# Kernel optimization log

Hardware: AMD Instinct MI355X
Metric: run time of the kernel (lower is better)

## Reference

```python
import jax, jax.numpy as jnp
import numpy as np

B, L, D_IN, D_MODEL, H = 8, 1024, 256, 512, 8
D_HEAD = D_MODEL // H


def setup_inputs() -> dict:
    key = jax.random.key(0)
    ks = jax.random.split(key, 12)
    queries = jax.random.normal(ks[0], (B, L, D_IN), dtype=jnp.float32)
    keys_ = jax.random.normal(ks[1], (B, L, D_IN), dtype=jnp.float32)
    values = jax.random.normal(ks[2], (B, L, D_IN), dtype=jnp.float32)
    attention_mask = jnp.ones((B, L), dtype=jnp.int32)
    # binary symmetric-ish adjacency (sparse molecular graph style)
    adjacency_matrix = (jax.random.uniform(ks[3], (B, L, L)) < 0.05).astype(jnp.float32)
    distance_matrix = jax.random.uniform(ks[4], (B, L, L), dtype=jnp.float32) * 10.0
    s = 1.0 / np.sqrt(D_IN)
    W_q = jax.random.normal(ks[5], (D_MODEL, D_IN), dtype=jnp.float32) * s
    W_k = jax.random.normal(ks[6], (D_MODEL, D_IN), dtype=jnp.float32) * s
    W_v = jax.random.normal(ks[7], (D_MODEL, D_IN), dtype=jnp.float32) * s
    W_o = jax.random.normal(ks[8], (D_MODEL, D_MODEL), dtype=jnp.float32) / np.sqrt(D_MODEL)
    lambda_a = jax.random.normal(ks[9], (H,), dtype=jnp.float32) * 0.1
    lambda_d = jax.random.normal(ks[10], (H,), dtype=jnp.float32) * 0.1
    return {"queries": queries, "keys": keys_, "values": values,
            "attention_mask": attention_mask, "adjacency_matrix": adjacency_matrix,
            "distance_matrix": distance_matrix, "W_q": W_q, "W_k": W_k,
            "W_v": W_v, "W_o": W_o, "lambda_a": lambda_a, "lambda_d": lambda_d}


def _split_heads(x):
    # (b, l, d_model) -> (b, h, l, d_head)
    b, l, _ = x.shape
    return x.reshape(b, l, H, D_HEAD).transpose(0, 2, 1, 3)


def reference(queries, keys, values, attention_mask, adjacency_matrix,
              distance_matrix, W_q, W_k, W_v, W_o, lambda_a, lambda_d):
    Q = _split_heads(queries @ W_q.T)   # (b,h,l,d)
    K = _split_heads(keys @ W_k.T)
    V = _split_heads(values @ W_v.T)
    scores = jnp.einsum("bhqd,bhkd->bhqk", Q, K) / jnp.sqrt(jnp.asarray(D_HEAD, Q.dtype))
    # MSRSA: per-head learned scalars inject graph structure into the scores
    scores = (scores
              + lambda_a[None, :, None, None] * adjacency_matrix[:, None, :, :]
              + lambda_d[None, :, None, None] * distance_matrix[:, None, :, :])
    mask = attention_mask[:, None, None, :] > 0  # (b,1,1,l) key mask
    scores = jnp.where(mask, scores, jnp.asarray(-1e9, scores.dtype))
    attn_weight = jax.nn.softmax(scores, axis=-1)  # (b,h,l,l)
    out = jnp.einsum("bhqk,bhkd->bhqd", attn_weight, V)
    out = out.transpose(0, 2, 1, 3).reshape(queries.shape[0], queries.shape[1], D_MODEL)
    return out @ W_o.T
```

## Files before the change

### kernel.cpp

```cpp
#include <hip/hip_runtime.h>
#include <hip/hip_fp16.h>

#define BB 8
#define LL 1024
#define DIN 256
#define DM 512
#define HH 8
#define DH 64

typedef __attribute__((ext_vector_type(8))) short bf16x8;
typedef __attribute__((ext_vector_type(4))) float f32x4;
typedef _Float16 h2f __attribute__((ext_vector_type(2)));

__device__ __forceinline__ unsigned short f2bf(float f) {
  union { float f; unsigned u; } c; c.f = f;
  unsigned u = c.u;
  return (unsigned short)((u + 0x7fffu + ((u >> 16) & 1u)) >> 16);
}

#if defined(__has_builtin)
#if __has_builtin(__builtin_amdgcn_cvt_pk_bf16_f32)
#define HAS_PK_BF16 1
#endif
#endif

#if defined(HAS_PK_BF16)
typedef __bf16 bf2 __attribute__((ext_vector_type(2)));
__device__ __forceinline__ unsigned pk2(float lo, float hi) {
  union { bf2 v; unsigned u; } c;
  c.v = __builtin_amdgcn_cvt_pk_bf16_f32(lo, hi);
  return c.u;
}
#else
__device__ __forceinline__ unsigned pk2(float lo, float hi) {
  return ((unsigned)f2bf(hi) << 16) | f2bf(lo);
}
#endif

__device__ __forceinline__ float biasdot(unsigned u, h2f lam, float t) {
#if defined(__HIP_DEVICE_COMPILE__)
  union { unsigned v; h2f hv; } c; c.v = u;
  return __builtin_amdgcn_fdot2(c.hv, lam, t, false);
#else
  (void)u; (void)lam;
  return t;
#endif
}

__device__ __forceinline__ unsigned pkh(float a, float d) {
  return (unsigned)__half_as_ushort(__float2half_rn(a)) |
         ((unsigned)__half_as_ushort(__float2half_rn(d)) << 16);
}

__device__ __forceinline__ void async_copy16(void* lds, const void* g) {
  __builtin_amdgcn_global_load_lds(
      (const __attribute__((address_space(1))) unsigned*)g,
      (__attribute__((address_space(3))) unsigned*)lds, 16, 0, 0);
}

__global__ __launch_bounds__(256) void prep(
    const float* __restrict__ qin, const float* __restrict__ kin,
    const float* __restrict__ vin,
    const float* __restrict__ wq, const float* __restrict__ wk,
    const float* __restrict__ wv, const float* __restrict__ wo,
    const int* __restrict__ msk,
    const float* __restrict__ adj, const float* __restrict__ dis,
    unsigned short* __restrict__ xq, unsigned short* __restrict__ xk,
    unsigned short* __restrict__ xv,
    unsigned short* __restrict__ wqb, unsigned short* __restrict__ wkb,
    unsigned short* __restrict__ wvb, unsigned short* __restrict__ wob,
    float* __restrict__ mad, unsigned* __restrict__ bp)
{
  int t = blockIdx.x * 256 + threadIdx.x;
  const int XS = 524288, WS = 32768;
  if (t < 3 * XS) {
    int seg = t >> 19, off = t & (XS - 1);
    const float* s = (seg == 0) ? qin : (seg == 1) ? kin : vin;
    unsigned short* d = (seg == 0) ? xq : (seg == 1) ? xk : xv;
    float4 f = ((const float4*)s)[off];
    uint2 o = { pk2(f.x, f.y), pk2(f.z, f.w) };
    ((uint2*)d)[off] = o;
    return;
  }
  t -= 3 * XS;
  if (t < 3 * WS) {
    int seg = t >> 15, off = t & (WS - 1);
    const float* s = (seg == 0) ? wq : (seg == 1) ? wk : wv;
    unsigned short* d = (seg == 0) ? wqb : (seg == 1) ? wkb : wvb;
    float4 f = ((const float4*)s)[off];
    uint2 o = { pk2(f.x, f.y), pk2(f.z, f.w) };
    ((uint2*)d)[off] = o;
    return;
  }
  t -= 3 * WS;
  if (t < 65536) {
    float4 f = ((const float4*)wo)[t];
    uint2 o = { pk2(f.x, f.y), pk2(f.z, f.w) };
    ((uint2*)wob)[t] = o;
    return;
  }
  t -= 65536;
  if (t < 2048) {
    int4 m = ((const int4*)msk)[t];
    float4 f = { m.x ? 0.0f : -30000.0f, m.y ? 0.0f : -30000.0f,
                 m.z ? 0.0f : -30000.0f, m.w ? 0.0f : -30000.0f };
    ((float4*)mad)[t] = f;
    return;
  }
  t -= 2048;
  float4 a4 = ((const float4*)adj)[t];
  float4 d4 = ((const float4*)dis)[t];
  uint4 o = { pkh(a4.x, d4.x), pkh(a4.y, d4.y), pkh(a4.z, d4.z), pkh(a4.w, d4.w) };
  ((uint4*)bp)[t] = o;
}

__global__ __launch_bounds__(256) void qkv_proj(
    const unsigned short* __restrict__ xq, const unsigned short* __restrict__ xk,
    const unsigned short* __restrict__ xv,
    const unsigned short* __restrict__ wqb, const unsigned short* __restrict__ wkb,
    const unsigned short* __restrict__ wvb,
    unsigned short* __restrict__ qb, unsigned short* __restrict__ kb,
    unsigned short* __restrict__ vt)
{
  const int t = blockIdx.z;
  const unsigned short* __restrict__ X = (t == 0) ? xq : (t == 1) ? xk : xv;
  const unsigned short* __restrict__ W = (t == 0) ? wqb : (t == 1) ? wkb : wvb;
  const int m0 = blockIdx.y * 128;
  const int h  = blockIdx.x;
  __shared__ __align__(16) char arena[24576];
  const int tid = threadIdx.x;
  const int wid = tid >> 6;
  const int lane = tid & 63;
  const int lo = lane & 15;
  const int quad = lane >> 4;

  f32x4 acc[2][4];
#pragma unroll
  for (int mi = 0; mi < 2; ++mi)
#pragma unroll
    for (int ni = 0; ni < 4; ++ni) acc[mi][ni] = (f32x4)0.0f;

#pragma unroll
  for (int j = 0; j < 2; ++j) {
    int id = j * 256 + tid, r = id >> 2, c = id & 3;
    async_copy16(arena + j * 4096 + wid * 1024,
                 X + (size_t)(m0 + r) * DIN + ((c ^ (r & 3)) * 8));
  }
  {
    int id = tid, r = id >> 2, c = id & 3;
    async_copy16(arena + 16384 + wid * 1024,
                 W + (size_t)(h * 64 + r) * DIN + ((c ^ (r & 3)) * 8));
  }
  __syncthreads();

  for (int it = 0; it < 8; ++it) {
    const int p = it & 1;
    if (it < 7) {
      const int kk = (it + 1) * 32, q = 1 - p;
#pragma unroll
      for (int j = 0; j < 2; ++j) {
        int id = j * 256 + tid, r = id >> 2, c = id & 3;
        async_copy16(arena + q * 8192 + j * 4096 + wid * 1024,
                     X + (size_t)(m0 + r) * DIN + kk + ((c ^ (r & 3)) * 8));
      }
      {
        int id = tid, r = id >> 2, c = id & 3;
        async_copy16(arena + 16384 + q * 4096 + wid * 1024,
                     W + (size_t)(h * 64 + r) * DIN + kk + ((c ^ (r & 3)) * 8));
      }
    }
    const unsigned short* Ab = (const unsigned short*)(arena + p * 8192);
    const unsigned short* Bb = (const unsigned short*)(arena + 16384 + p * 4096);
    bf16x8 a[2], bfr[4];
#pragma unroll
    for (int mi = 0; mi < 2; ++mi) {
      int R = wid * 32 + mi * 16 + lo;
      a[mi] = *(const bf16x8*)&Ab[R * 32 + ((quad ^ (R & 3)) * 8)];
    }
#pragma unroll
    for (int ni = 0; ni < 4; ++ni) {
      int N = ni * 16 + lo;
      bfr[ni] = *(const bf16x8*)&Bb[N * 32 + ((quad ^ (N & 3)) * 8)];
    }
#pragma unroll
    for (int mi = 0; mi < 2; ++mi)
#pragma unroll
      for (int ni = 0; ni < 4; ++ni)
        acc[mi][ni] = __builtin_amdgcn_mfma_f32_16x16x32_bf16(
            a[mi], bfr[ni], acc[mi][ni], 0, 0, 0);
    __syncthreads();
  }

  const int b = m0 >> 10;
  const int lbase0 = (m0 & 1023) + wid * 32;
  if (t < 2) {
    unsigned short* dstp = (t == 0) ? qb : kb;
#pragma unroll
    for (int mi = 0; mi < 2; ++mi)
#pragma unroll
      for (int ni = 0; ni < 4; ++ni) {
        int d = ni * 16 + lo;
#pragma unroll
        for (int r = 0; r < 4; ++r) {
          int lb = lbase0 + mi * 16 + quad * 4 + r;
          dstp[((size_t)(b * HH + h) * LL + lb) * DH + d] = f2bf(acc[mi][ni][r]);
        }
      }
  } else {
#pragma unroll
    for (int mi = 0; mi < 2; ++mi)
#pragma unroll
      for (int ni = 0; ni < 4; ++ni) {
        int d = ni * 16 + lo;
        int lb = lbase0 + mi * 16 + quad * 4;
        uint2 o = { pk2(acc[mi][ni][0], acc[mi][ni][1]),
                    pk2(acc[mi][ni][2], acc[mi][ni][3]) };
        *(uint2*)&vt[((size_t)(b * HH + h) * DH + d) * LL + lb] = o;
      }
  }
}

__global__ __launch_bounds__(256, 3) void attn(
    const unsigned short* __restrict__ qb, const unsigned short* __restrict__ kb,
    const unsigned short* __restrict__ vt,
    const float* __restrict__ mad, const unsigned* __restrict__ bp,
    const float* __restrict__ la_, const float* __restrict__ ld_,
    unsigned short* __restrict__ ao)
{
  const int bi = blockIdx.x;
  const int b  = bi & 7;
  const int hg = (bi >> 3) & 3;
  const int q0 = (bi >> 5) * 32;
  const int tid = threadIdx.x;
  const int wid = tid >> 6;
  const int lane = tid & 63;
  const int lo = lane & 15;
  const int quad = lane >> 4;
  const int h  = hg * 2 + (wid & 1);
  const int kh = wid >> 1;
  const int bh = b * HH + h;

  __shared__ __align__(16) char arena[17408];
  unsigned short* pbufw = (unsigned short*)arena + wid * 1280;
  float*          mgbuf = (float*)arena;

  const float LOG2E = 1.44269504f;
  const float la2 = la_[h] * LOG2E, ld2 = ld_[h] * LOG2E;
  const float sc2 = 0.125f * LOG2E;
  h2f lam2;
  lam2.x = (_Float16)la2;
  lam2.y = (_Float16)ld2;

  const unsigned short* qp = qb + ((size_t)bh * LL + q0) * DH;
  bf16x8 qB[2][2];
#pragma unroll
  for (int nj = 0; nj < 2; ++nj)
#pragma unroll
    for (int ki = 0; ki < 2; ++ki)
      qB[nj][ki] = *(const bf16x8*)&qp[(nj * 16 + lo) * DH + ki * 32 + quad * 8];

  const unsigned short* kp = kb + (size_t)bh * LL * DH;
  const unsigned short* vp = vt + (size_t)bh * DH * LL;
  const unsigned* bpp = bp + ((size_t)b * LL + q0) * LL;
  const float* mp = mad + b * LL;

  f32x4 o[4][2];
  float rs[2] = {0.0f, 0.0f};
#pragma unroll
  for (int md = 0; md < 4; ++md)
#pragma unroll
    for (int nj = 0; nj < 2; ++nj) o[md][nj] = (f32x4)0.0f;

  const int kbeg = kh * (LL / 2);

  bf16x8 kA0[2][2], kA1[2][2];
#pragma unroll
  for (int mi = 0; mi < 2; ++mi)
#pragma unroll
    for (int ki = 0; ki < 2; ++ki)
      kA0[mi][ki] = *(const bf16x8*)&kp[(size_t)(kbeg + mi * 16 + lo) * DH +
                                        ki * 32 + quad * 8];

#define ATTN_TILE(KC, KN, JT)                                                  \
  do {                                                                         \
    const int k0 = kbeg + (JT) * 32;                                           \
    const int kn0 = ((JT) < 15) ? (k0 + 32) : k0;   \
    uint4 ub[2][2];                                                            \
    _Pragma("unroll") for (int mi = 0; mi < 2; ++mi)                           \
      _Pragma("unroll") for (int nj = 0; nj < 2; ++nj)                         \
        ub[mi][nj] = *(const uint4*)&bpp[(size_t)(nj * 16 + lo) * LL +         \
                                         k0 + mi * 16 + quad * 4];             \
    f32x4 msv[2];                                                              \
    _Pragma("unroll") for (int mi = 0; mi < 2; ++mi)                           \
      msv[mi] = *(const f32x4*)&mp[k0 + mi * 16 + quad * 4];                   \
    bf16x8 vA[4];                                                              \
    _Pragma("unroll") for (int md = 0; md < 4; ++md)                           \
      vA[md] = *(const bf16x8*)&vp[(md * 16 + lo) * LL + k0 + quad * 8];       \
    _Pragma("unroll") for (int mi = 0; mi < 2; ++mi)                           \
      _Pragma("unroll") for (int ki = 0; ki < 2; ++ki)                         \
        KN[mi][ki] = *(const bf16x8*)&kp[(size_t)(kn0 + mi * 16 + lo) * DH +   \
                                         ki * 32 + quad * 8];                  \
    __builtin_amdgcn_sched_barrier(0);           \
    f32x4 s[2][2];                                                             \
    _Pragma("unroll") for (int mi = 0; mi < 2; ++mi)                           \
      _Pragma("unroll") for (int nj = 0; nj < 2; ++nj) s[mi][nj] = (f32x4)0.0f;\
    _Pragma("unroll") for (int ki = 0; ki < 2; ++ki)                           \
      _Pragma("unroll") for (int mi = 0; mi < 2; ++mi)                         \
        _Pragma("unroll") for (int nj = 0; nj < 2; ++nj)                       \
          s[mi][nj] = __builtin_amdgcn_mfma_f32_16x16x32_bf16(                 \
              KC[mi][ki], qB[nj][ki], s[mi][nj], 0, 0, 0);                     \
    _Pragma("unroll") for (int mi = 0; mi < 2; ++mi)                           \
      _Pragma("unroll") for (int nj = 0; nj < 2; ++nj) {                       \
        float p4[4];                                                           \
        _Pragma("unroll") for (int r = 0; r < 4; ++r) {                        \
          float tb = fmaf(s[mi][nj][r], sc2, msv[mi][r]);                      \
          p4[r] = __builtin_amdgcn_exp2f(biasdot(ub[mi][nj][r], lam2, tb));    \
        }                                                                      \
        rs[nj] += (p4[0] + p4[1]) + (p4[2] + p4[3]);                           \
        uint2 w = { pk2(p4[0], p4[1]), pk2(p4[2], p4[3]) };                    \
        *(uint2*)&pbufw[(nj * 16 + lo) * 40 + mi * 16 + quad * 4] = w;         \
      }                                                                        \
    asm volatile("s_waitcnt lgkmcnt(0)" ::: "memory");                         \
    bf16x8 pB[2];                                                              \
    _Pragma("unroll") for (int nj = 0; nj < 2; ++nj)                           \
      pB[nj] = *(const bf16x8*)&pbufw[(nj * 16 + lo) * 40 + quad * 8];         \
    _Pragma("unroll") for (int md = 0; md < 4; ++md)                           \
      _Pragma("unroll") for (int nj = 0; nj < 2; ++nj)                         \
        o[md][nj] = __builtin_amdgcn_mfma_f32_16x16x32_bf16(                   \
            vA[md], pB[nj], o[md][nj], 0, 0, 0);                               \
  } while (0)

  for (int j2 = 0; j2 < 8; ++j2) {
    ATTN_TILE(kA0, kA1, 2 * j2);
    ATTN_TILE(kA1, kA0, 2 * j2 + 1);
  }
#undef ATTN_TILE

  __syncthreads();
  const int hs = wid & 1;
  if (kh == 1) {
#pragma unroll
    for (int md = 0; md < 4; ++md)
#pragma unroll
      for (int nj = 0; nj < 2; ++nj)
#pragma unroll
        for (int r = 0; r < 4; ++r)
          mgbuf[hs * 2176 + ((md * 2 + nj) * 4 + r) * 64 + lane] = o[md][nj][r];
    mgbuf[hs * 2176 + 32 * 64 + lane] = rs[0];
    mgbuf[hs * 2176 + 33 * 64 + lane] = rs[1];
  }
  __syncthreads();
  if (kh == 0) {
#pragma unroll
    for (int md = 0; md < 4; ++md)
#pragma unroll
      for (int nj = 0; nj < 2; ++nj)
#pragma unroll
        for (int r = 0; r < 4; ++r)
          o[md][nj][r] += mgbuf[hs * 2176 + ((md * 2 + nj) * 4 + r) * 64 + lane];
    rs[0] += mgbuf[hs * 2176 + 32 * 64 + lane];
    rs[1] += mgbuf[hs * 2176 + 33 * 64 + lane];
    float inv[2];
#pragma unroll
    for (int nj = 0; nj < 2; ++nj) {
      rs[nj] += __shfl_xor(rs[nj], 16);
      rs[nj] += __shfl_xor(rs[nj], 32);
      inv[nj] = __builtin_amdgcn_rcpf(rs[nj]);
    }
#pragma unroll
    for (int md = 0; md < 4; ++md)
#pragma unroll
      for (int nj = 0; nj < 2; ++nj) {
        int l = q0 + nj * 16 + lo;
        uint2 st = { pk2(o[md][nj][0] * inv[nj], o[md][nj][1] * inv[nj]),
                     pk2(o[md][nj][2] * inv[nj], o[md][nj][3] * inv[nj]) };
        *(uint2*)&ao[((size_t)b * LL + l) * DM + h * DH + md * 16 + quad * 4] = st;
      }
  }
}

__global__ __launch_bounds__(256) void oproj(
    const unsigned short* __restrict__ ao, const unsigned short* __restrict__ wob,
    float* __restrict__ out)
{
  const int m0 = blockIdx.y * 128;
  const int n0 = blockIdx.x * 64;
  __shared__ __align__(16) char arena[24576];
  const int tid = threadIdx.x;
  const int wid = tid >> 6;
  const int lane = tid & 63;
  const int lo = lane & 15;
  const int quad = lane >> 4;

  f32x4 acc[2][4];
#pragma unroll
  for (int mi = 0; mi < 2; ++mi)
#pragma unroll
    for (int ni = 0; ni < 4; ++ni) acc[mi][ni] = (f32x4)0.0f;

#pragma unroll
  for (int j = 0; j < 2; ++j) {
    int id = j * 256 + tid, r = id >> 2, c = id & 3;
    async_copy16(arena + j * 4096 + wid * 1024,
                 ao + (size_t)(m0 + r) * DM + ((c ^ (r & 3)) * 8));
  }
  {
    int id = tid, r = id >> 2, c = id & 3;
    async_copy16(arena + 16384 + wid * 1024,
                 wob + (size_t)(n0 + r) * DM + ((c ^ (r & 3)) * 8));
  }
  __syncthreads();

  for (int it = 0; it < 16; ++it) {
    const int p = it & 1;
    if (it < 15) {
      const int kk = (it + 1) * 32, q = 1 - p;
#pragma unroll
      for (int j = 0; j < 2; ++j) {
        int id = j * 256 + tid, r = id >> 2, c = id & 3;
        async_copy16(arena + q * 8192 + j * 4096 + wid * 1024,
                     ao + (size_t)(m0 + r) * DM + kk + ((c ^ (r & 3)) * 8));
      }
      {
        int id = tid, r = id >> 2, c = id & 3;
        async_copy16(arena + 16384 + q * 4096 + wid * 1024,
                     wob + (size_t)(n0 + r) * DM + kk + ((c ^ (r & 3)) * 8));
      }
    }
    const unsigned short* Ab = (const unsigned short*)(arena + p * 8192);
    const unsigned short* Bb = (const unsigned short*)(arena + 16384 + p * 4096);
    bf16x8 a[2], bfr[4];
#pragma unroll
    for (int mi = 0; mi < 2; ++mi) {
      int R = wid * 32 + mi * 16 + lo;
      a[mi] = *(const bf16x8*)&Ab[R * 32 + ((quad ^ (R & 3)) * 8)];
    }
#pragma unroll
    for (int ni = 0; ni < 4; ++ni) {
      int N = ni * 16 + lo;
      bfr[ni] = *(const bf16x8*)&Bb[N * 32 + ((quad ^ (N & 3)) * 8)];
    }
#pragma unroll
    for (int mi = 0; mi < 2; ++mi)
#pragma unroll
      for (int ni = 0; ni < 4; ++ni)
        acc[mi][ni] = __builtin_amdgcn_mfma_f32_16x16x32_bf16(
            a[mi], bfr[ni], acc[mi][ni], 0, 0, 0);
    __syncthreads();
  }

#pragma unroll
  for (int mi = 0; mi < 2; ++mi)
#pragma unroll
    for (int ni = 0; ni < 4; ++ni)
#pragma unroll
      for (int r = 0; r < 4; ++r)
        out[(size_t)(m0 + wid * 32 + mi * 16 + quad * 4 + r) * DM +
            n0 + ni * 16 + lo] = acc[mi][ni][r];
}

extern "C" void kernel_launch(void* const* d_in, const int* in_sizes, int n_in,
                              void* d_out, int out_size, void* d_ws, size_t ws_size,
                              hipStream_t stream) {
  const float* qin = (const float*)d_in[0];
  const float* kin = (const float*)d_in[1];
  const float* vin = (const float*)d_in[2];
  const int*   msk = (const int*)d_in[3];
  const float* adj = (const float*)d_in[4];
  const float* dis = (const float*)d_in[5];
  const float* wq  = (const float*)d_in[6];
  const float* wk  = (const float*)d_in[7];
  const float* wv  = (const float*)d_in[8];
  const float* wo  = (const float*)d_in[9];
  const float* la  = (const float*)d_in[10];
  const float* ld  = (const float*)d_in[11];
  float* out = (float*)d_out;

  const size_t tensb = (size_t)BB * HH * LL * DH;
  const size_t xsz   = (size_t)BB * LL * DIN;
  unsigned short* qb  = (unsigned short*)d_ws;
  unsigned short* kb  = qb + tensb;
  unsigned short* vt  = kb + tensb;
  unsigned short* ao  = vt + tensb;
  unsigned short* xq  = ao;
  unsigned short* xk  = ao + xsz;
  unsigned short* xv  = ao + tensb;
  unsigned short* wqb = xv + xsz;
  unsigned short* wkb = wqb + (size_t)DM * DIN;
  unsigned short* wvb = wkb + (size_t)DM * DIN;
  unsigned short* wob = wvb + (size_t)DM * DIN;
  float*          mdd = (float*)(wob + (size_t)DM * DM);
  unsigned*       bpk = (unsigned*)(mdd + (size_t)BB * LL);

  prep<<<dim3(14984), 256, 0, stream>>>(qin, kin, vin, wq, wk, wv, wo, msk,
                                        adj, dis,
                                        xq, xk, xv, wqb, wkb, wvb, wob, mdd, bpk);
  qkv_proj<<<dim3(8, 64, 3), 256, 0, stream>>>(xq, xk, xv, wqb, wkb, wvb, qb, kb, vt);
  attn<<<dim3(1024), 256, 0, stream>>>(qb, kb, vt, mdd, bpk, la, ld, ao);
  oproj<<<dim3(8, 64), 256, 0, stream>>>(ao, wob, out);
}
```

Before: 276.7 us.

## Stage bias tiles in LDS via async double-buffered copies shared across head pair

The packed adjacency/distance bias tile, which both heads in a block read, is now loaded once per key-half through async global-to-LDS copies into a swizzled double buffer, prefetching the next tile while the current one is processed. Each wave then reads the bias from LDS instead of issuing its own global loads. V loads are moved after the QK MFMAs, the sched_barrier is removed, and occupancy in launch bounds is raised to 4. The cost is a __syncthreads per tile, plus extra LDS use that may limit occupancy.

```diff
diff --git a/kernel.cpp b/kernel.cpp
--- a/kernel.cpp
+++ b/kernel.cpp
@@ -220,7 +220,7 @@
   }
 }
 
-__global__ __launch_bounds__(256, 3) void attn(
+__global__ __launch_bounds__(256, 4) void attn(
     const unsigned short* __restrict__ qb, const unsigned short* __restrict__ kb,
     const unsigned short* __restrict__ vt,
     const float* __restrict__ mad, const unsigned* __restrict__ bp,
@@ -240,8 +240,8 @@
   const int kh = wid >> 1;
   const int bh = b * HH + h;
 
-  __shared__ __align__(16) char arena[17408];
-  unsigned short* pbufw = (unsigned short*)arena + wid * 1280;
+  __shared__ __align__(16) char arena[26624];
+  unsigned short* pbufw = (unsigned short*)(arena + 16384) + wid * 1280;
   float*          mgbuf = (float*)arena;
 
   const float LOG2E = 1.44269504f;
@@ -272,7 +272,16 @@
     for (int nj = 0; nj < 2; ++nj) o[md][nj] = (f32x4)0.0f;
 
   const int kbeg = kh * (LL / 2);
-
+  const int r8 = lane >> 3, p8 = lane & 7;
+
+  if ((wid & 1) == 0) {
+    const int khs = wid >> 1;
+    const unsigned* bg = bpp + khs * (LL / 2);
+#pragma unroll
+    for (int j = 0; j < 4; ++j)
+      async_copy16(arena + khs * 4096 + j * 1024,
+                   bg + (size_t)(j * 8 + r8) * LL + ((p8 ^ r8) * 4));
+  }
   bf16x8 kA0[2][2], kA1[2][2];
 #pragma unroll
   for (int mi = 0; mi < 2; ++mi)
@@ -280,27 +289,29 @@
     for (int ki = 0; ki < 2; ++ki)
       kA0[mi][ki] = *(const bf16x8*)&kp[(size_t)(kbeg + mi * 16 + lo) * DH +
                                         ki * 32 + quad * 8];
+  __syncthreads();
 
 #define ATTN_TILE(KC, KN, JT)                                                  \
   do {                                                                         \
+    const int p = (JT) & 1;                                                    \
     const int k0 = kbeg + (JT) * 32;                                           \
-    const int kn0 = ((JT) < 15) ? (k0 + 32) : k0;   \
-    uint4 ub[2][2];                                                            \
-    _Pragma("unroll") for (int mi = 0; mi < 2; ++mi)                           \
-      _Pragma("unroll") for (int nj = 0; nj < 2; ++nj)                         \
-        ub[mi][nj] = *(const uint4*)&bpp[(size_t)(nj * 16 + lo) * LL +         \
-                                         k0 + mi * 16 + quad * 4];             \
+    if ((JT) < 15) {                                                           \
+      if ((wid & 1) == 0) {                                                    \
+        const int khs = wid >> 1;                                              \
+        const unsigned* bg = bpp + khs * (LL / 2) + ((JT) + 1) * 32;           \
+        _Pragma("unroll") for (int j = 0; j < 4; ++j)                          \
+          async_copy16(arena + (1 - p) * 8192 + khs * 4096 + j * 1024,         \
+                       bg + (size_t)(j * 8 + r8) * LL + ((p8 ^ r8) * 4));      \
+      }                                                                        \
+      const unsigned short* kg = kp + (size_t)(k0 + 32) * DH;                  \
+      _Pragma("unroll") for (int mi = 0; mi < 2; ++mi)                         \
+        _Pragma("unroll") for (int ki = 0; ki < 2; ++ki)                       \
+          KN[mi][ki] = *(const bf16x8*)&kg[(mi * 16 + lo) * DH +               \
+                                           ki * 32 + quad * 8];                \
+    }                                                                          \
     f32x4 msv[2];                                                              \
     _Pragma("unroll") for (int mi = 0; mi < 2; ++mi)                           \
       msv[mi] = *(const f32x4*)&mp[k0 + mi * 16 + quad * 4];                   \
-    bf16x8 vA[4];                                                              \
-    _Pragma("unroll") for (int md = 0; md < 4; ++md)                           \
-      vA[md] = *(const bf16x8*)&vp[(md * 16 + lo) * LL + k0 + quad * 8];       \
-    _Pragma("unroll") for (int mi = 0; mi < 2; ++mi)                           \
-      _Pragma("unroll") for (int ki = 0; ki < 2; ++ki)                         \
-        KN[mi][ki] = *(const bf16x8*)&kp[(size_t)(kn0 + mi * 16 + lo) * DH +   \
-                                         ki * 32 + quad * 8];                  \
-    __builtin_amdgcn_sched_barrier(0);           \
     f32x4 s[2][2];                                                             \
     _Pragma("unroll") for (int mi = 0; mi < 2; ++mi)                           \
       _Pragma("unroll") for (int nj = 0; nj < 2; ++nj) s[mi][nj] = (f32x4)0.0f;\
@@ -309,12 +320,18 @@
         _Pragma("unroll") for (int nj = 0; nj < 2; ++nj)                       \
           s[mi][nj] = __builtin_amdgcn_mfma_f32_16x16x32_bf16(                 \
               KC[mi][ki], qB[nj][ki], s[mi][nj], 0, 0, 0);                     \
+    bf16x8 vA[4];                                                              \
+    _Pragma("unroll") for (int md = 0; md < 4; ++md)                           \
+      vA[md] = *(const bf16x8*)&vp[(md * 16 + lo) * LL + k0 + quad * 8];       \
+    const unsigned* bbf = (const unsigned*)(arena + p * 8192) + kh * 1024;     \
     _Pragma("unroll") for (int mi = 0; mi < 2; ++mi)                           \
       _Pragma("unroll") for (int nj = 0; nj < 2; ++nj) {                       \
+        uint4 u = *(const uint4*)&bbf[(nj * 16 + lo) * 32 +                    \
+                                      (((mi * 4 + quad) ^ (lo & 7)) * 4)];     \
         float p4[4];                                                           \
         _Pragma("unroll") for (int r = 0; r < 4; ++r) {                        \
           float tb = fmaf(s[mi][nj][r], sc2, msv[mi][r]);                      \
-          p4[r] = __builtin_amdgcn_exp2f(biasdot(ub[mi][nj][r], lam2, tb));    \
+          p4[r] = __builtin_amdgcn_exp2f(biasdot(u[r], lam2, tb));             \
         }                                                                      \
         rs[nj] += (p4[0] + p4[1]) + (p4[2] + p4[3]);                           \
         uint2 w = { pk2(p4[0], p4[1]), pk2(p4[2], p4[3]) };                    \
@@ -328,6 +345,7 @@
       _Pragma("unroll") for (int nj = 0; nj < 2; ++nj)                         \
         o[md][nj] = __builtin_amdgcn_mfma_f32_16x16x32_bf16(                   \
             vA[md], pB[nj], o[md][nj], 0, 0, 0);                               \
+    __syncthreads();                                                           \
   } while (0)
 
   for (int j2 = 0; j2 < 8; ++j2) {
@@ -336,7 +354,6 @@
   }
 #undef ATTN_TILE
 
-  __syncthreads();
   const int hs = wid & 1;
   if (kh == 1) {
 #pragma unroll
```

Result: slower. 317.8 us (+14.9%).

## Stage K tiles via async LDS copies and keep P in registers

Applied to the files above, without the earlier changes.

K tiles are now double-buffered into a per-wave swizzled LDS region with async global-to-LDS copies, and the bias tile is prefetched one step ahead instead of being loaded each tile. The P matrix no longer round-trips through LDS. The V-transpose store permutes its key order to match the P register layout, which avoids the LDS shuffle. This removes an LDS write/wait/read per tile and hides K and bias load latency, at the cost of a larger LDS arena (32KB), dropped occupancy hint in launch bounds, and hand-tuned vmcnt waits that must match the issue order.

```diff
diff --git a/kernel.cpp b/kernel.cpp
--- a/kernel.cpp
+++ b/kernel.cpp
@@ -212,7 +212,7 @@
 #pragma unroll
       for (int ni = 0; ni < 4; ++ni) {
         int d = ni * 16 + lo;
-        int lb = lbase0 + mi * 16 + quad * 4;
+        int lb = lbase0 + quad * 8 + mi * 4;
         uint2 o = { pk2(acc[mi][ni][0], acc[mi][ni][1]),
                     pk2(acc[mi][ni][2], acc[mi][ni][3]) };
         *(uint2*)&vt[((size_t)(b * HH + h) * DH + d) * LL + lb] = o;
@@ -220,7 +220,7 @@
   }
 }
 
-__global__ __launch_bounds__(256, 3) void attn(
+__global__ __launch_bounds__(256) void attn(
     const unsigned short* __restrict__ qb, const unsigned short* __restrict__ kb,
     const unsigned short* __restrict__ vt,
     const float* __restrict__ mad, const unsigned* __restrict__ bp,
@@ -240,9 +240,9 @@
   const int kh = wid >> 1;
   const int bh = b * HH + h;
 
-  __shared__ __align__(16) char arena[17408];
-  unsigned short* pbufw = (unsigned short*)arena + wid * 1280;
-  float*          mgbuf = (float*)arena;
+  __shared__ __align__(16) char arena[32768];
+  char* kpriv = arena + wid * 8192;
+  float* mgbuf = (float*)arena;
 
   const float LOG2E = 1.44269504f;
   const float la2 = la_[h] * LOG2E, ld2 = ld_[h] * LOG2E;
@@ -272,35 +272,54 @@
     for (int nj = 0; nj < 2; ++nj) o[md][nj] = (f32x4)0.0f;
 
   const int kbeg = kh * (LL / 2);
-
-  bf16x8 kA0[2][2], kA1[2][2];
+  const int r8 = lane >> 3, p8 = lane & 7;
+
+  uint4 ub0[2][2], ub1[2][2];
 #pragma unroll
   for (int mi = 0; mi < 2; ++mi)
 #pragma unroll
-    for (int ki = 0; ki < 2; ++ki)
-      kA0[mi][ki] = *(const bf16x8*)&kp[(size_t)(kbeg + mi * 16 + lo) * DH +
-                                        ki * 32 + quad * 8];
-
-#define ATTN_TILE(KC, KN, JT)                                                  \
+    for (int nj = 0; nj < 2; ++nj)
+      ub0[mi][nj] = *(const uint4*)&bpp[(size_t)(nj * 16 + lo) * LL +
+                                        kbeg + mi * 16 + quad * 4];
+  asm volatile("" ::: "memory");
+  {
+    const unsigned short* kg = kp + (size_t)kbeg * DH;
+#pragma unroll
+    for (int j = 0; j < 4; ++j)
+      async_copy16(kpriv + j * 1024, kg + (j * 8 + r8) * 64 + ((p8 ^ r8) * 8));
+  }
+
+#define ATTN_TILE(UBC, UBN, JT)                                                \
   do {                                                                         \
+    const int p = (JT) & 1;                                                    \
     const int k0 = kbeg + (JT) * 32;                                           \
-    const int kn0 = ((JT) < 15) ? (k0 + 32) : k0;   \
-    uint4 ub[2][2];                                                            \
-    _Pragma("unroll") for (int mi = 0; mi < 2; ++mi)                           \
-      _Pragma("unroll") for (int nj = 0; nj < 2; ++nj)                         \
-        ub[mi][nj] = *(const uint4*)&bpp[(size_t)(nj * 16 + lo) * LL +         \
-                                         k0 + mi * 16 + quad * 4];             \
+    bf16x8 vA[4];                                                              \
+    _Pragma("unroll") for (int md = 0; md < 4; ++md)                           \
+      vA[md] = *(const bf16x8*)&vp[(md * 16 + lo) * LL + k0 + quad * 8];       \
     f32x4 msv[2];                                                              \
     _Pragma("unroll") for (int mi = 0; mi < 2; ++mi)                           \
       msv[mi] = *(const f32x4*)&mp[k0 + mi * 16 + quad * 4];                   \
-    bf16x8 vA[4];                                                              \
-    _Pragma("unroll") for (int md = 0; md < 4; ++md)                           \
-      vA[md] = *(const bf16x8*)&vp[(md * 16 + lo) * LL + k0 + quad * 8];       \
+    asm volatile("" ::: "memory");          \
+    if ((JT) < 15) {                                                           \
+      _Pragma("unroll") for (int mi = 0; mi < 2; ++mi)                         \
+        _Pragma("unroll") for (int nj = 0; nj < 2; ++nj)                       \
+          UBN[mi][nj] = *(const uint4*)&bpp[(size_t)(nj * 16 + lo) * LL +      \
+                                            k0 + 32 + mi * 16 + quad * 4];     \
+      const unsigned short* kg = kp + (size_t)(k0 + 32) * DH;                  \
+      _Pragma("unroll") for (int j = 0; j < 4; ++j)                            \
+        async_copy16(kpriv + (1 - p) * 4096 + j * 1024,                        \
+                     kg + (j * 8 + r8) * 64 + ((p8 ^ r8) * 8));                \
+      asm volatile("" ::: "memory");                                           \
+      asm volatile("s_waitcnt vmcnt(14)" ::: "memory");      \
+    } else {                                                                   \
+      asm volatile("s_waitcnt vmcnt(6)" ::: "memory");                         \
+    }                                                                          \
+    const unsigned short* kbf = (const unsigned short*)(kpriv + p * 4096);     \
+    bf16x8 kA[2][2];                                                           \
     _Pragma("unroll") for (int mi = 0; mi < 2; ++mi)                           \
       _Pragma("unroll") for (int ki = 0; ki < 2; ++ki)                         \
-        KN[mi][ki] = *(const bf16x8*)&kp[(size_t)(kn0 + mi * 16 + lo) * DH +   \
-                                         ki * 32 + quad * 8];                  \
-    __builtin_amdgcn_sched_barrier(0);           \
+        kA[mi][ki] = *(const bf16x8*)&kbf[(mi * 16 + lo) * 64 +                \
+                                          (((ki * 4 + quad) ^ (lo & 7)) * 8)]; \
     f32x4 s[2][2];                                                             \
     _Pragma("unroll") for (int mi = 0; mi < 2; ++mi)                           \
       _Pragma("unroll") for (int nj = 0; nj < 2; ++nj) s[mi][nj] = (f32x4)0.0f;\
@@ -308,22 +327,26 @@
       _Pragma("unroll") for (int mi = 0; mi < 2; ++mi)                         \
         _Pragma("unroll") for (int nj = 0; nj < 2; ++nj)                       \
           s[mi][nj] = __builtin_amdgcn_mfma_f32_16x16x32_bf16(                 \
-              KC[mi][ki], qB[nj][ki], s[mi][nj], 0, 0, 0);                     \
+              kA[mi][ki], qB[nj][ki], s[mi][nj], 0, 0, 0);                     \
+    unsigned pw[2][4];                                                         \
     _Pragma("unroll") for (int mi = 0; mi < 2; ++mi)                           \
       _Pragma("unroll") for (int nj = 0; nj < 2; ++nj) {                       \
         float p4[4];                                                           \
         _Pragma("unroll") for (int r = 0; r < 4; ++r) {                        \
           float tb = fmaf(s[mi][nj][r], sc2, msv[mi][r]);                      \
-          p4[r] = __builtin_amdgcn_exp2f(biasdot(ub[mi][nj][r], lam2, tb));    \
+          p4[r] = __builtin_amdgcn_exp2f(biasdot(UBC[mi][nj][r], lam2, tb));   \
         }                                                                      \
         rs[nj] += (p4[0] + p4[1]) + (p4[2] + p4[3]);                           \
-        uint2 w = { pk2(p4[0], p4[1]), pk2(p4[2], p4[3]) };                    \
-        *(uint2*)&pbufw[(nj * 16 + lo) * 40 + mi * 16 + quad * 4] = w;         \
+        pw[nj][mi * 2]     = pk2(p4[0], p4[1]);                                \
+        pw[nj][mi * 2 + 1] = pk2(p4[2], p4[3]);                                \
       }                                                                        \
-    asm volatile("s_waitcnt lgkmcnt(0)" ::: "memory");                         \
     bf16x8 pB[2];                                                              \
-    _Pragma("unroll") for (int nj = 0; nj < 2; ++nj)                           \
-      pB[nj] = *(const bf16x8*)&pbufw[(nj * 16 + lo) * 40 + quad * 8];         \
+    _Pragma("unroll") for (int nj = 0; nj < 2; ++nj) {                         \
+      union { unsigned u[4]; bf16x8 v; } pc;                                   \
+      pc.u[0] = pw[nj][0]; pc.u[1] = pw[nj][1];                                \
+      pc.u[2] = pw[nj][2]; pc.u[3] = pw[nj][3];                                \
+      pB[nj] = pc.v;                                                           \
+    }                                                                          \
     _Pragma("unroll") for (int md = 0; md < 4; ++md)                           \
       _Pragma("unroll") for (int nj = 0; nj < 2; ++nj)                         \
         o[md][nj] = __builtin_amdgcn_mfma_f32_16x16x32_bf16(                   \
@@ -331,8 +354,8 @@
   } while (0)
 
   for (int j2 = 0; j2 < 8; ++j2) {
-    ATTN_TILE(kA0, kA1, 2 * j2);
-    ATTN_TILE(kA1, kA0, 2 * j2 + 1);
+    ATTN_TILE(ub0, ub1, 2 * j2);
+    ATTN_TILE(ub1, ub0, 2 * j2 + 1);
   }
 #undef ATTN_TILE
 
```

After: 250.2 us. 1.11x faster.
